# Optimization experiments

Measured on AMD Instinct MI355X. Metric: run time of the kernel, lower is better.

Reference implementation:

```python
import jax, jax.numpy as jnp
from jax import lax
import numpy as np

V, E, H, L = 512, 512, 1024, 2
B, T = 128, 512
PAD = 0


def _uniform(k, shape, bound):
    return jax.random.uniform(k, shape, jnp.float32, -bound, bound)


def setup_inputs() -> dict:
    key = jax.random.key(0)
    ks = jax.random.split(key, 14)
    kH = 1.0 / np.sqrt(H)
    inp = {
        'seq': jax.random.randint(ks[0], (B, T), 0, V, dtype=jnp.int32),
        'seq_lens': jax.random.randint(ks[1], (B,), 1, T + 1, dtype=jnp.int32),
        'teacher_p': jnp.asarray(0.5, jnp.float32),
        'embeds': jax.random.normal(ks[2], (V, E), jnp.float32),
        # layer 0: input size E; layer 1: input size H (PyTorch gate order i,f,g,o)
        'W_ih0': _uniform(ks[3], (4 * H, E), kH),
        'W_hh0': _uniform(ks[4], (4 * H, H), kH),
        'b_ih0': _uniform(ks[5], (4 * H,), kH),
        'b_hh0': _uniform(ks[6], (4 * H,), kH),
        'W_ih1': _uniform(ks[7], (4 * H, H), kH),
        'W_hh1': _uniform(ks[8], (4 * H, H), kH),
        'b_ih1': _uniform(ks[9], (4 * H,), kH),
        'b_hh1': _uniform(ks[10], (4 * H,), kH),
        'fc_w': _uniform(ks[11], (V, H), 1.0 / np.sqrt(H)),
        'fc_b': _uniform(ks[12], (V,), 1.0 / np.sqrt(H)),
    }
    return inp


def _lstm_cell(x, h, c, Wih, Whh, bih, bhh):
    g = x @ Wih.T + h @ Whh.T + (bih + bhh)  # [B, 4H]
    i, f, gg, o = jnp.split(g, 4, axis=-1)
    c = jax.nn.sigmoid(f) * c + jax.nn.sigmoid(i) * jnp.tanh(gg)
    h = jax.nn.sigmoid(o) * jnp.tanh(c)
    return h, c


def reference(seq, seq_lens, teacher_p, embeds, W_ih0, W_hh0, b_ih0, b_hh0,
              W_ih1, W_hh1, b_ih1, b_hh1, fc_w, fc_b):
    emb = embeds.at[PAD].set(0.0)  # padding_idx row is zero
    # pre-drawn teacher-forcing uniforms, one per (t, b)
    u = jax.random.uniform(jax.random.key(1), (T, B), jnp.float32)

    def step(carry, xs):
        h0, c0, h1, c1, prev_logits = carry
        tok_t, u_t, t = xs
        use_teacher = (t == 0) | (u_t < teacher_p)
        tok = jnp.where(use_teacher, tok_t, jnp.argmax(prev_logits, axis=1).astype(tok_t.dtype))
        x = emb[tok]  # [B, E]
        h0, c0 = _lstm_cell(x, h0, c0, W_ih0, W_hh0, b_ih0, b_hh0)
        h1, c1 = _lstm_cell(h0, h1, c1, W_ih1, W_hh1, b_ih1, b_hh1)
        logits = h1 @ fc_w.T + fc_b  # [B, V]
        return (h0, c0, h1, c1, logits), logits

    z = jnp.zeros((B, H), jnp.float32)
    init = (z, z, z, z, jnp.zeros((B, V), jnp.float32))
    xs = (seq.T, u, jnp.arange(T))
    _, logits = lax.scan(step, init, xs)  # [T, B, V]
    return jnp.transpose(logits, (1, 0, 2))  # [B, T, V]
```

## Files before the change

kernel.cpp:

```cpp
#include <hip/hip_runtime.h>
#include <cstdint>
#include <cstddef>

#define BB 128
#define TT 512
#define VV 512
#define EE 512
#define HH 1024
#define NBLK 256
#define BHS ((size_t)BB * HH)

__device__ __forceinline__ float tf_uniform(unsigned i) {
  unsigned x0 = 0u;
  unsigned x1 = i;
  const unsigned k0 = 0u, k1 = 1u, k2 = 0x1BD11BDBu;
  x0 += k0; x1 += k1;
#define ROTL_(v, r) (((v) << (r)) | ((v) >> (32 - (r))))
#define RND_(r) { x0 += x1; x1 = ROTL_(x1, (r)); x1 ^= x0; }
  RND_(13) RND_(15) RND_(26) RND_(6)   x0 += k1; x1 += k2 + 1u;
  RND_(17) RND_(29) RND_(16) RND_(24)  x0 += k2; x1 += k0 + 2u;
  RND_(13) RND_(15) RND_(26) RND_(6)   x0 += k0; x1 += k1 + 3u;
  RND_(17) RND_(29) RND_(16) RND_(24)  x0 += k1; x1 += k2 + 4u;
  RND_(13) RND_(15) RND_(26) RND_(6)   x0 += k2; x1 += k0 + 5u;
#undef RND_
#undef ROTL_
  unsigned bits = x0 ^ x1;
  unsigned fb = (bits >> 9) | 0x3f800000u;
  return __uint_as_float(fb) - 1.0f;
}

__device__ __forceinline__ void gridbar(unsigned* bar, unsigned target) {
  __syncthreads();
  if (threadIdx.x == 0) {
    __threadfence();
    __hip_atomic_fetch_add(bar, 1u, __ATOMIC_RELAXED, __HIP_MEMORY_SCOPE_AGENT);
    while (__hip_atomic_fetch_add(bar, 0u, __ATOMIC_RELAXED, __HIP_MEMORY_SCOPE_AGENT) < target) {
      __builtin_amdgcn_s_sleep(1);
    }
    __threadfence();
  }
  __syncthreads();
}

__global__ __launch_bounds__(256) void init_kernel(float* __restrict__ h0T,
                                                   float* __restrict__ c0T,
                                                   float* __restrict__ h1T,
                                                   float* __restrict__ c1T,
                                                   unsigned* __restrict__ bar) {
  int tid = blockIdx.x * 256 + threadIdx.x;
  if (tid == 0) *bar = 0u;
  if (tid < (int)BHS) {
    h0T[tid] = 0.f; c0T[tid] = 0.f; h1T[tid] = 0.f; c1T[tid] = 0.f;
  }
}

__global__ __launch_bounds__(256, 1) void lstm_persistent(
    const int* __restrict__ seq,
    const float* __restrict__ teacher_p,
    const float* __restrict__ emb,
    const float* __restrict__ Wih0, const float* __restrict__ Whh0,
    const float* __restrict__ bih0, const float* __restrict__ bhh0,
    const float* __restrict__ Wih1, const float* __restrict__ Whh1,
    const float* __restrict__ bih1, const float* __restrict__ bhh1,
    const float* __restrict__ fcw, const float* __restrict__ fcb,
    float* __restrict__ out,
    float* __restrict__ h0T, float* __restrict__ c0T,
    float* __restrict__ h1T, float* __restrict__ c1T,
    unsigned long long* __restrict__ fcpart,
    unsigned* __restrict__ bar) {
  __shared__ float Xs[32][132];
  __shared__ float Ws2[16][36];
  __shared__ float Xsf[64][36];
  __shared__ float Wsf[8][68];
  __shared__ int tok_s[BB];

  const int tid = threadIdx.x;
  const int bn  = blockIdx.x;
  const int ty  = tid >> 3;
  const int tx  = tid & 7;

  const float tp = teacher_p[0];

  float bc0[2][4], bc1[2][4];
#pragma unroll
  for (int r = 0; r < 2; ++r) {
    int j = (tid + (r << 8)) >> 7;
    int u = (bn << 2) + j;
#pragma unroll
    for (int g = 0; g < 4; ++g) {
      bc0[r][g] = bih0[g * HH + u] + bhh0[g * HH + u];
      bc1[r][g] = bih1[g * HH + u] + bhh1[g * HH + u];
    }
  }

  const int wc  = tid >> 3;
  const int wkq = tid & 7;
  const int gr  = (wc >> 2) * HH + (bn << 2) + (wc & 3);
  const float* wih0row = Wih0 + (size_t)gr * EE;
  const float* whh0row = Whh0 + (size_t)gr * HH;
  const float* wih1row = Wih1 + (size_t)gr * HH;
  const float* whh1row = Whh1 + (size_t)gr * HH;

  const int rb = bn >> 6, cb = bn & 63;
  const int fb = tid >> 3;
  const int fcc = tid & 7;
  const int fn = (cb << 3) + fcc;
  const float fcbr = fcb[fn];
  const float* fcwrow = fcw + (size_t)((cb << 3) + (tid >> 4)) * HH;

  unsigned target = 0;

  for (int t = 0; t < TT; ++t) {
    const float* h0r = h0T + (size_t)(t & 1) * BHS;
    float*       h0w = h0T + (size_t)((t + 1) & 1) * BHS;
    const float* h1r = h1T + (size_t)(t & 1) * BHS;
    float*       h1w = h1T + (size_t)((t + 1) & 1) * BHS;

    {
      int b = tid >> 1, h = tid & 1;
      unsigned long long best = 0ull;
      if (t > 0) {
        const unsigned long long* fp = fcpart + ((size_t)b << 6);
#pragma unroll 8
        for (int i = 0; i < 32; ++i) {
          unsigned long long k2 = fp[(i << 1) + h];
          if (k2 > best) best = k2;
        }
        unsigned long long o = __shfl_xor(best, 1);
        if (o > best) best = o;
      }
      if (h == 0) {
        int sel;
        if (t == 0) {
          sel = seq[(size_t)b * TT];
        } else {
          float uu = tf_uniform((unsigned)(t * BB + b));
          sel = (uu < tp) ? seq[(size_t)b * TT + t]
                          : (int)(0xFFFFFFFFu - (unsigned)(best & 0xFFFFFFFFull));
        }
        tok_s[b] = sel;
      }
    }
    __syncthreads();

    {
      float acc[4][2] = {{0.f,0.f},{0.f,0.f},{0.f,0.f},{0.f,0.f}};
      float4 x0, x1, x2, x3, w;

      auto pf = [&](int kt) {
        if (kt < 16) {
          const int kb = kt << 5;
          { int f=tid;     int b=f>>3, kq=f&7; int tk=tok_s[b];
            x0 = tk ? *(const float4*)(emb + ((size_t)tk<<9) + kb + (kq<<2)) : make_float4(0.f,0.f,0.f,0.f); }
          { int f=tid+256; int b=f>>3, kq=f&7; int tk=tok_s[b];
            x1 = tk ? *(const float4*)(emb + ((size_t)tk<<9) + kb + (kq<<2)) : make_float4(0.f,0.f,0.f,0.f); }
          { int f=tid+512; int b=f>>3, kq=f&7; int tk=tok_s[b];
            x2 = tk ? *(const float4*)(emb + ((size_t)tk<<9) + kb + (kq<<2)) : make_float4(0.f,0.f,0.f,0.f); }
          { int f=tid+768; int b=f>>3, kq=f&7; int tk=tok_s[b];
            x3 = tk ? *(const float4*)(emb + ((size_t)tk<<9) + kb + (kq<<2)) : make_float4(0.f,0.f,0.f,0.f); }
          if (tid < 128) w = *(const float4*)(wih0row + kb + (wkq<<2));
        } else {
          const float* src = h0r + ((size_t)(kt - 16) << 5) * BB;
          { int f=tid;     x0 = *(const float4*)(src + (f>>5)*BB + ((f&31)<<2)); }
          { int f=tid+256; x1 = *(const float4*)(src + (f>>5)*BB + ((f&31)<<2)); }
          { int f=tid+512; x2 = *(const float4*)(src + (f>>5)*BB + ((f&31)<<2)); }
          { int f=tid+768; x3 = *(const float4*)(src + (f>>5)*BB + ((f&31)<<2)); }
          if (tid < 128) w = *(const float4*)(whh0row + ((kt - 16) << 5) + (wkq<<2));
        }
      };
      auto st = [&](int kt) {
        if (kt < 16) {
          { int f=tid;     int b=f>>3, kk=(f&7)<<2; Xs[kk][b]=x0.x; Xs[kk+1][b]=x0.y; Xs[kk+2][b]=x0.z; Xs[kk+3][b]=x0.w; }
          { int f=tid+256; int b=f>>3, kk=(f&7)<<2; Xs[kk][b]=x1.x; Xs[kk+1][b]=x1.y; Xs[kk+2][b]=x1.z; Xs[kk+3][b]=x1.w; }
          { int f=tid+512; int b=f>>3, kk=(f&7)<<2; Xs[kk][b]=x2.x; Xs[kk+1][b]=x2.y; Xs[kk+2][b]=x2.z; Xs[kk+3][b]=x2.w; }
          { int f=tid+768; int b=f>>3, kk=(f&7)<<2; Xs[kk][b]=x3.x; Xs[kk+1][b]=x3.y; Xs[kk+2][b]=x3.z; Xs[kk+3][b]=x3.w; }
        } else {
          { int f=tid;     *(float4*)&Xs[f>>5][(f&31)<<2] = x0; }
          { int f=tid+256; *(float4*)&Xs[f>>5][(f&31)<<2] = x1; }
          { int f=tid+512; *(float4*)&Xs[f>>5][(f&31)<<2] = x2; }
          { int f=tid+768; *(float4*)&Xs[f>>5][(f&31)<<2] = x3; }
        }
        if (tid < 128) *(float4*)&Ws2[wc][wkq<<2] = w;
      };

      pf(0);
      for (int kt = 0; kt < 48; ++kt) {
        st(kt);
        __syncthreads();
        if (kt < 47) pf(kt + 1);
#pragma unroll
        for (int k4 = 0; k4 < 8; ++k4) {
          float w0[4], w1[4];
          *(float4*)w0 = *(const float4*)&Ws2[tx << 1][k4 << 2];
          *(float4*)w1 = *(const float4*)&Ws2[(tx << 1) + 1][k4 << 2];
#pragma unroll
          for (int kk = 0; kk < 4; ++kk) {
            float a[4];
            *(float4*)a = *(const float4*)&Xs[(k4 << 2) + kk][ty << 2];
#pragma unroll
            for (int i = 0; i < 4; ++i) {
              acc[i][0] = fmaf(a[i], w0[kk], acc[i][0]);
              acc[i][1] = fmaf(a[i], w1[kk], acc[i][1]);
            }
          }
        }
        __syncthreads();
      }

      float* gbuf = &Xs[0][0];
#pragma unroll
      for (int i = 0; i < 4; ++i) {
        int r = (ty << 2) + i;
        gbuf[r * 17 + (tx << 1)]     = acc[i][0];
        gbuf[r * 17 + (tx << 1) + 1] = acc[i][1];
      }
      __syncthreads();
#pragma unroll
      for (int r = 0; r < 2; ++r) {
        int idx = tid + (r << 8);
        int b = idx & 127, j = idx >> 7;
        float gi = gbuf[b * 17 + j]      + bc0[r][0];
        float gf = gbuf[b * 17 + 4 + j]  + bc0[r][1];
        float gg = gbuf[b * 17 + 8 + j]  + bc0[r][2];
        float go = gbuf[b * 17 + 12 + j] + bc0[r][3];
        float i_ = 1.f / (1.f + expf(-gi));
        float f_ = 1.f / (1.f + expf(-gf));
        float g_ = tanhf(gg);
        float o_ = 1.f / (1.f + expf(-go));
        size_t off = ((size_t)((bn << 2) + j)) * BB + b;
        float cn = f_ * c0T[off] + i_ * g_;
        c0T[off] = cn;
        h0w[off] = o_ * tanhf(cn);
      }
    }
    target += NBLK; gridbar(bar, target);

    {
      float acc[4][2] = {{0.f,0.f},{0.f,0.f},{0.f,0.f},{0.f,0.f}};
      float4 x0, x1, x2, x3, w;

      auto pf2 = [&](int kt) {
        const float* src = (kt < 32) ? (h0w + ((size_t)kt << 5) * BB)
                                     : (h1r + ((size_t)(kt - 32) << 5) * BB);
        { int f=tid;     x0 = *(const float4*)(src + (f>>5)*BB + ((f&31)<<2)); }
        { int f=tid+256; x1 = *(const float4*)(src + (f>>5)*BB + ((f&31)<<2)); }
        { int f=tid+512; x2 = *(const float4*)(src + (f>>5)*BB + ((f&31)<<2)); }
        { int f=tid+768; x3 = *(const float4*)(src + (f>>5)*BB + ((f&31)<<2)); }
        if (tid < 128) {
          w = (kt < 32) ? *(const float4*)(wih1row + (kt << 5) + (wkq<<2))
                        : *(const float4*)(whh1row + ((kt - 32) << 5) + (wkq<<2));
        }
      };
      auto st2 = [&]() {
        { int f=tid;     *(float4*)&Xs[f>>5][(f&31)<<2] = x0; }
        { int f=tid+256; *(float4*)&Xs[f>>5][(f&31)<<2] = x1; }
        { int f=tid+512; *(float4*)&Xs[f>>5][(f&31)<<2] = x2; }
        { int f=tid+768; *(float4*)&Xs[f>>5][(f&31)<<2] = x3; }
        if (tid < 128) *(float4*)&Ws2[wc][wkq<<2] = w;
      };

      pf2(0);
      for (int kt = 0; kt < 64; ++kt) {
        st2();
        __syncthreads();
        if (kt < 63) pf2(kt + 1);
#pragma unroll
        for (int k4 = 0; k4 < 8; ++k4) {
          float w0[4], w1[4];
          *(float4*)w0 = *(const float4*)&Ws2[tx << 1][k4 << 2];
          *(float4*)w1 = *(const float4*)&Ws2[(tx << 1) + 1][k4 << 2];
#pragma unroll
          for (int kk = 0; kk < 4; ++kk) {
            float a[4];
            *(float4*)a = *(const float4*)&Xs[(k4 << 2) + kk][ty << 2];
#pragma unroll
            for (int i = 0; i < 4; ++i) {
              acc[i][0] = fmaf(a[i], w0[kk], acc[i][0]);
              acc[i][1] = fmaf(a[i], w1[kk], acc[i][1]);
            }
          }
        }
        __syncthreads();
      }

      float* gbuf = &Xs[0][0];
#pragma unroll
      for (int i = 0; i < 4; ++i) {
        int r = (ty << 2) + i;
        gbuf[r * 17 + (tx << 1)]     = acc[i][0];
        gbuf[r * 17 + (tx << 1) + 1] = acc[i][1];
      }
      __syncthreads();
#pragma unroll
      for (int r = 0; r < 2; ++r) {
        int idx = tid + (r << 8);
        int b = idx & 127, j = idx >> 7;
        float gi = gbuf[b * 17 + j]      + bc1[r][0];
        float gf = gbuf[b * 17 + 4 + j]  + bc1[r][1];
        float gg = gbuf[b * 17 + 8 + j]  + bc1[r][2];
        float go = gbuf[b * 17 + 12 + j] + bc1[r][3];
        float i_ = 1.f / (1.f + expf(-gi));
        float f_ = 1.f / (1.f + expf(-gf));
        float g_ = tanhf(gg);
        float o_ = 1.f / (1.f + expf(-go));
        size_t off = ((size_t)((bn << 2) + j)) * BB + b;
        float cn = f_ * c1T[off] + i_ * g_;
        c1T[off] = cn;
        h1w[off] = o_ * tanhf(cn);
      }
    }
    target += NBLK; gridbar(bar, target);

    {
      float facc = 0.f;
      float4 y0, y1, fw;
      auto pf3 = [&](int kt) {
        const float* src = h1w + ((size_t)kt << 6) * BB + ((size_t)rb << 5);
        { int f=tid;     y0 = *(const float4*)(src + (f>>3)*BB + ((f&7)<<2)); }
        { int f=tid+256; y1 = *(const float4*)(src + (f>>3)*BB + ((f&7)<<2)); }
        if (tid < 128) fw = *(const float4*)(fcwrow + (kt << 6) + ((tid & 15) << 2));
      };
      auto st3 = [&]() {
        { int f=tid;     *(float4*)&Xsf[f>>3][(f&7)<<2] = y0; }
        { int f=tid+256; *(float4*)&Xsf[f>>3][(f&7)<<2] = y1; }
        if (tid < 128) *(float4*)&Wsf[tid >> 4][(tid & 15) << 2] = fw;
      };
      pf3(0);
      for (int kt = 0; kt < 16; ++kt) {
        st3();
        __syncthreads();
        if (kt < 15) pf3(kt + 1);
#pragma unroll
        for (int k = 0; k < 64; ++k)
          facc = fmaf(Xsf[k][fb], Wsf[fcc][k], facc);
        __syncthreads();
      }
      int b = (rb << 5) + fb;
      float lg = facc + fcbr;
      out[((size_t)b * TT + t) * VV + fn] = lg;
      unsigned sbits = __float_as_uint(lg);
      sbits = (sbits & 0x80000000u) ? ~sbits : (sbits | 0x80000000u);
      unsigned long long key = ((unsigned long long)sbits << 32) |
                               (unsigned long long)(0xFFFFFFFFu - (unsigned)fn);
#pragma unroll
      for (int off = 4; off > 0; off >>= 1) {
        unsigned long long o = __shfl_down(key, off, 8);
        if (o > key) key = o;
      }
      if (fcc == 0) fcpart[((size_t)b << 6) + cb] = key;
    }
    target += NBLK; gridbar(bar, target);
  }
}

extern "C" void kernel_launch(void* const* d_in, const int* in_sizes, int n_in,
                              void* d_out, int out_size, void* d_ws, size_t ws_size,
                              hipStream_t stream) {
  const int*   seq       = (const int*)d_in[0];
  const float* teacher_p = (const float*)d_in[2];
  const float* embeds    = (const float*)d_in[3];
  const float* W_ih0     = (const float*)d_in[4];
  const float* W_hh0     = (const float*)d_in[5];
  const float* b_ih0     = (const float*)d_in[6];
  const float* b_hh0     = (const float*)d_in[7];
  const float* W_ih1     = (const float*)d_in[8];
  const float* W_hh1     = (const float*)d_in[9];
  const float* b_ih1     = (const float*)d_in[10];
  const float* b_hh1     = (const float*)d_in[11];
  const float* fc_w      = (const float*)d_in[12];
  const float* fc_b      = (const float*)d_in[13];
  float* out = (float*)d_out;

  char* ws = (char*)d_ws;
  float* h0T = (float*)(ws);
  float* c0T = (float*)(ws + 2 * BHS * 4);
  float* h1T = (float*)(ws + 3 * BHS * 4);
  float* c1T = (float*)(ws + 5 * BHS * 4);
  unsigned long long* fcpart = (unsigned long long*)(ws + 6 * BHS * 4);
  unsigned* bar = (unsigned*)(ws + 6 * BHS * 4 + 65536);

  init_kernel<<<512, 256, 0, stream>>>(h0T, c0T, h1T, c1T, bar);

  void* args[] = {
    (void*)&seq, (void*)&teacher_p, (void*)&embeds,
    (void*)&W_ih0, (void*)&W_hh0, (void*)&b_ih0, (void*)&b_hh0,
    (void*)&W_ih1, (void*)&W_hh1, (void*)&b_ih1, (void*)&b_hh1,
    (void*)&fc_w, (void*)&fc_b, (void*)&out,
    (void*)&h0T, (void*)&c0T, (void*)&h1T, (void*)&c1T,
    (void*)&fcpart, (void*)&bar
  };
  hipError_t err = hipLaunchCooperativeKernel((void*)lstm_persistent,
                                              dim3(NBLK), dim3(256), args, 0, stream);
  if (err != hipSuccess) {
    lstm_persistent<<<dim3(NBLK), dim3(256), 0, stream>>>(
        seq, teacher_p, embeds, W_ih0, W_hh0, b_ih0, b_hh0,
        W_ih1, W_hh1, b_ih1, b_hh1, fc_w, fc_b, out,
        h0T, c0T, h1T, c1T, fcpart, bar);
  }
}
```

Baseline: 108.1 ms.

## Keep LSTM and FC weights register-resident in persistent kernel, stream activations

Each block now loads its slice of the gate and FC weight matrices into registers once before the time loop. Per step it streams only the batch activations through shared memory in row-major layout, with a split-K dot-product across warps reduced by shuffles and shared-memory partials. This removes the re-reading of roughly 40MB of weights from memory on every timestep. Block size goes to 512 threads, which raises register pressure (about 128 float registers for weights) and risks spills or lower occupancy.

```diff
diff --git a/kernel.cpp b/kernel.cpp
--- a/kernel.cpp
+++ b/kernel.cpp
@@ -8,6 +8,7 @@
 #define EE 512
 #define HH 1024
 #define NBLK 256
+#define NTHR 512
 #define BHS ((size_t)BB * HH)
 
 __device__ __forceinline__ float tf_uniform(unsigned i) {
@@ -29,6 +30,8 @@
   return __uint_as_float(fb) - 1.0f;
 }
 
+__device__ __forceinline__ float4 ld4(const float* p) { return *(const float4*)(p); }
+
 __device__ __forceinline__ void gridbar(unsigned* bar, unsigned target) {
   __syncthreads();
   if (threadIdx.x == 0) {
@@ -42,19 +45,14 @@
   __syncthreads();
 }
 
-__global__ __launch_bounds__(256) void init_kernel(float* __restrict__ h0T,
-                                                   float* __restrict__ c0T,
-                                                   float* __restrict__ h1T,
-                                                   float* __restrict__ c1T,
+__global__ __launch_bounds__(256) void init_kernel(float* __restrict__ wsf,
                                                    unsigned* __restrict__ bar) {
-  int tid = blockIdx.x * 256 + threadIdx.x;
+  size_t tid = (size_t)blockIdx.x * 256 + threadIdx.x;
   if (tid == 0) *bar = 0u;
-  if (tid < (int)BHS) {
-    h0T[tid] = 0.f; c0T[tid] = 0.f; h1T[tid] = 0.f; c1T[tid] = 0.f;
-  }
+  if (tid < 6 * BHS) wsf[tid] = 0.f;
 }
 
-__global__ __launch_bounds__(256, 1) void lstm_persistent(
+__global__ __launch_bounds__(NTHR, 2) void lstm_persistent(
     const int* __restrict__ seq,
     const float* __restrict__ teacher_p,
     const float* __restrict__ emb,
@@ -64,50 +62,60 @@
     const float* __restrict__ bih1, const float* __restrict__ bhh1,
     const float* __restrict__ fcw, const float* __restrict__ fcb,
     float* __restrict__ out,
-    float* __restrict__ h0T, float* __restrict__ c0T,
-    float* __restrict__ h1T, float* __restrict__ c1T,
+    float* __restrict__ h0T, float* __restrict__ c0,
+    float* __restrict__ h1T, float* __restrict__ c1,
     unsigned long long* __restrict__ fcpart,
     unsigned* __restrict__ bar) {
-  __shared__ float Xs[32][132];
-  __shared__ float Ws2[16][36];
-  __shared__ float Xsf[64][36];
-  __shared__ float Wsf[8][68];
-  __shared__ int tok_s[BB];
-
-  const int tid = threadIdx.x;
-  const int bn  = blockIdx.x;
-  const int ty  = tid >> 3;
-  const int tx  = tid & 7;
-
+  __shared__ float xbuf[8704];
+  __shared__ float gacc[BB][17];
+  __shared__ float scr[8][4][17];
+  __shared__ int   tok_s[BB];
+
+  const int tid   = threadIdx.x;
+  const int bn    = blockIdx.x;
+  const int w     = tid >> 6;
+  const int lane  = tid & 63;
+  const int c16   = lane & 15;
+  const int squad = lane >> 4;
+  const int s32   = (w << 2) | squad;
+  const int c8    = lane & 7;
+  const int oct   = lane >> 3;
+  const int s64   = (w << 3) | oct;
+  const int grow  = (c16 >> 2) * HH + (bn << 2) + (c16 & 3);
+  const int rb    = bn & 3, cb = bn >> 2;
+  const int ucell = (bn << 2) + (tid & 3);
+
+  float4 w0r[12], w1r[16], wfr[4];
+  {
+    const int k0 = s32 * 48;
+#pragma unroll
+    for (int q = 0; q < 12; ++q) {
+      int k = k0 + (q << 2);
+      w0r[q] = (k < EE) ? ld4(Wih0 + (size_t)grow * EE + k)
+                        : ld4(Whh0 + (size_t)grow * HH + (k - EE));
+    }
+  }
+  {
+    const int k0 = s32 * 64;
+#pragma unroll
+    for (int q = 0; q < 16; ++q) {
+      int k = k0 + (q << 2);
+      w1r[q] = (k < HH) ? ld4(Wih1 + (size_t)grow * HH + k)
+                        : ld4(Whh1 + (size_t)grow * HH + (k - HH));
+    }
+  }
+  {
+    const float* wrow = fcw + (size_t)((cb << 3) + c8) * HH + s64 * 16;
+#pragma unroll
+    for (int q = 0; q < 4; ++q) wfr[q] = ld4(wrow + (q << 2));
+  }
+  float bc0[4], bc1[4];
+#pragma unroll
+  for (int g = 0; g < 4; ++g) {
+    bc0[g] = bih0[g * HH + ucell] + bhh0[g * HH + ucell];
+    bc1[g] = bih1[g * HH + ucell] + bhh1[g * HH + ucell];
+  }
   const float tp = teacher_p[0];
-
-  float bc0[2][4], bc1[2][4];
-#pragma unroll
-  for (int r = 0; r < 2; ++r) {
-    int j = (tid + (r << 8)) >> 7;
-    int u = (bn << 2) + j;
-#pragma unroll
-    for (int g = 0; g < 4; ++g) {
-      bc0[r][g] = bih0[g * HH + u] + bhh0[g * HH + u];
-      bc1[r][g] = bih1[g * HH + u] + bhh1[g * HH + u];
-    }
-  }
-
-  const int wc  = tid >> 3;
-  const int wkq = tid & 7;
-  const int gr  = (wc >> 2) * HH + (bn << 2) + (wc & 3);
-  const float* wih0row = Wih0 + (size_t)gr * EE;
-  const float* whh0row = Whh0 + (size_t)gr * HH;
-  const float* wih1row = Wih1 + (size_t)gr * HH;
-  const float* whh1row = Whh1 + (size_t)gr * HH;
-
-  const int rb = bn >> 6, cb = bn & 63;
-  const int fb = tid >> 3;
-  const int fcc = tid & 7;
-  const int fn = (cb << 3) + fcc;
-  const float fcbr = fcb[fn];
-  const float* fcwrow = fcw + (size_t)((cb << 3) + (tid >> 4)) * HH;
-
   unsigned target = 0;
 
   for (int t = 0; t < TT; ++t) {
@@ -117,19 +125,21 @@
     float*       h1w = h1T + (size_t)((t + 1) & 1) * BHS;
 
     {
-      int b = tid >> 1, h = tid & 1;
+      int b = tid >> 2, qd = tid & 3;
       unsigned long long best = 0ull;
       if (t > 0) {
         const unsigned long long* fp = fcpart + ((size_t)b << 6);
-#pragma unroll 8
-        for (int i = 0; i < 32; ++i) {
-          unsigned long long k2 = fp[(i << 1) + h];
+#pragma unroll 4
+        for (int i = 0; i < 16; ++i) {
+          unsigned long long k2 = fp[(i << 2) + qd];
           if (k2 > best) best = k2;
         }
-        unsigned long long o = __shfl_xor(best, 1);
-        if (o > best) best = o;
-      }
-      if (h == 0) {
+        unsigned long long o1 = __shfl_xor(best, 1);
+        if (o1 > best) best = o1;
+        unsigned long long o2 = __shfl_xor(best, 2);
+        if (o2 > best) best = o2;
+      }
+      if (qd == 0) {
         int sel;
         if (t == 0) {
           sel = seq[(size_t)b * TT];
@@ -144,210 +154,225 @@
     __syncthreads();
 
     {
-      float acc[4][2] = {{0.f,0.f},{0.f,0.f},{0.f,0.f},{0.f,0.f}};
-      float4 x0, x1, x2, x3, w;
-
-      auto pf = [&](int kt) {
-        if (kt < 16) {
-          const int kb = kt << 5;
-          { int f=tid;     int b=f>>3, kq=f&7; int tk=tok_s[b];
-            x0 = tk ? *(const float4*)(emb + ((size_t)tk<<9) + kb + (kq<<2)) : make_float4(0.f,0.f,0.f,0.f); }
-          { int f=tid+256; int b=f>>3, kq=f&7; int tk=tok_s[b];
-            x1 = tk ? *(const float4*)(emb + ((size_t)tk<<9) + kb + (kq<<2)) : make_float4(0.f,0.f,0.f,0.f); }
-          { int f=tid+512; int b=f>>3, kq=f&7; int tk=tok_s[b];
-            x2 = tk ? *(const float4*)(emb + ((size_t)tk<<9) + kb + (kq<<2)) : make_float4(0.f,0.f,0.f,0.f); }
-          { int f=tid+768; int b=f>>3, kq=f&7; int tk=tok_s[b];
-            x3 = tk ? *(const float4*)(emb + ((size_t)tk<<9) + kb + (kq<<2)) : make_float4(0.f,0.f,0.f,0.f); }
-          if (tid < 128) w = *(const float4*)(wih0row + kb + (wkq<<2));
-        } else {
-          const float* src = h0r + ((size_t)(kt - 16) << 5) * BB;
-          { int f=tid;     x0 = *(const float4*)(src + (f>>5)*BB + ((f&31)<<2)); }
-          { int f=tid+256; x1 = *(const float4*)(src + (f>>5)*BB + ((f&31)<<2)); }
-          { int f=tid+512; x2 = *(const float4*)(src + (f>>5)*BB + ((f&31)<<2)); }
-          { int f=tid+768; x3 = *(const float4*)(src + (f>>5)*BB + ((f&31)<<2)); }
-          if (tid < 128) w = *(const float4*)(whh0row + ((kt - 16) << 5) + (wkq<<2));
-        }
-      };
-      auto st = [&](int kt) {
-        if (kt < 16) {
-          { int f=tid;     int b=f>>3, kk=(f&7)<<2; Xs[kk][b]=x0.x; Xs[kk+1][b]=x0.y; Xs[kk+2][b]=x0.z; Xs[kk+3][b]=x0.w; }
-          { int f=tid+256; int b=f>>3, kk=(f&7)<<2; Xs[kk][b]=x1.x; Xs[kk+1][b]=x1.y; Xs[kk+2][b]=x1.z; Xs[kk+3][b]=x1.w; }
-          { int f=tid+512; int b=f>>3, kk=(f&7)<<2; Xs[kk][b]=x2.x; Xs[kk+1][b]=x2.y; Xs[kk+2][b]=x2.z; Xs[kk+3][b]=x2.w; }
-          { int f=tid+768; int b=f>>3, kk=(f&7)<<2; Xs[kk][b]=x3.x; Xs[kk+1][b]=x3.y; Xs[kk+2][b]=x3.z; Xs[kk+3][b]=x3.w; }
-        } else {
-          { int f=tid;     *(float4*)&Xs[f>>5][(f&31)<<2] = x0; }
-          { int f=tid+256; *(float4*)&Xs[f>>5][(f&31)<<2] = x1; }
-          { int f=tid+512; *(float4*)&Xs[f>>5][(f&31)<<2] = x2; }
-          { int f=tid+768; *(float4*)&Xs[f>>5][(f&31)<<2] = x3; }
-        }
-        if (tid < 128) *(float4*)&Ws2[wc][wkq<<2] = w;
-      };
-
-      pf(0);
-      for (int kt = 0; kt < 48; ++kt) {
-        st(kt);
-        __syncthreads();
-        if (kt < 47) pf(kt + 1);
-#pragma unroll
-        for (int k4 = 0; k4 < 8; ++k4) {
-          float w0[4], w1[4];
-          *(float4*)w0 = *(const float4*)&Ws2[tx << 1][k4 << 2];
-          *(float4*)w1 = *(const float4*)&Ws2[(tx << 1) + 1][k4 << 2];
-#pragma unroll
-          for (int kk = 0; kk < 4; ++kk) {
-            float a[4];
-            *(float4*)a = *(const float4*)&Xs[(k4 << 2) + kk][ty << 2];
-#pragma unroll
-            for (int i = 0; i < 4; ++i) {
-              acc[i][0] = fmaf(a[i], w0[kk], acc[i][0]);
-              acc[i][1] = fmaf(a[i], w1[kk], acc[i][1]);
-            }
+      float4 sg[3];
+      auto loadP1 = [&](int bt) {
+#pragma unroll
+        for (int i = 0; i < 3; ++i) {
+          int u = tid + (i << 9);
+          int row = u / 384;
+          int k = (u - row * 384) << 2;
+          int b = (bt << 2) + row;
+          float4 v;
+          if (k < EE) {
+            int tk = tok_s[b];
+            v = tk ? ld4(emb + (size_t)tk * EE + k) : make_float4(0.f, 0.f, 0.f, 0.f);
+          } else {
+            v = ld4(h0r + (size_t)b * HH + (k - EE));
           }
-        }
-        __syncthreads();
-      }
-
-      float* gbuf = &Xs[0][0];
-#pragma unroll
-      for (int i = 0; i < 4; ++i) {
-        int r = (ty << 2) + i;
-        gbuf[r * 17 + (tx << 1)]     = acc[i][0];
-        gbuf[r * 17 + (tx << 1) + 1] = acc[i][1];
-      }
-      __syncthreads();
-#pragma unroll
-      for (int r = 0; r < 2; ++r) {
-        int idx = tid + (r << 8);
-        int b = idx & 127, j = idx >> 7;
-        float gi = gbuf[b * 17 + j]      + bc0[r][0];
-        float gf = gbuf[b * 17 + 4 + j]  + bc0[r][1];
-        float gg = gbuf[b * 17 + 8 + j]  + bc0[r][2];
-        float go = gbuf[b * 17 + 12 + j] + bc0[r][3];
+          sg[i] = v;
+        }
+      };
+      auto writeP1 = [&]() {
+#pragma unroll
+        for (int i = 0; i < 3; ++i) {
+          int u = tid + (i << 9);
+          int row = u / 384;
+          int k = (u - row * 384) << 2;
+          int dst = row * 1664 + (k / 48) * 52 + (k % 48);
+          *(float4*)(xbuf + dst) = sg[i];
+        }
+      };
+      loadP1(0); writeP1(); __syncthreads();
+      for (int bt = 0; bt < 32; ++bt) {
+        if (bt < 31) loadP1(bt + 1);
+        const float* xp0 = xbuf + s32 * 52;
+#pragma unroll 2
+        for (int r = 0; r < 4; ++r) {
+          const float* xp = xp0 + r * 1664;
+          float a0 = 0.f, a1 = 0.f, a2 = 0.f, a3 = 0.f;
+#pragma unroll
+          for (int q = 0; q < 12; ++q) {
+            float4 xv = *(const float4*)(xp + (q << 2));
+            a0 = fmaf(xv.x, w0r[q].x, a0);
+            a1 = fmaf(xv.y, w0r[q].y, a1);
+            a2 = fmaf(xv.z, w0r[q].z, a2);
+            a3 = fmaf(xv.w, w0r[q].w, a3);
+          }
+          float acc = (a0 + a1) + (a2 + a3);
+          acc += __shfl_xor(acc, 16);
+          acc += __shfl_xor(acc, 32);
+          if (squad == 0) scr[w][r][c16] = acc;
+        }
+        __syncthreads();
+        if (tid < 64) {
+          int r = tid >> 4, c = tid & 15;
+          float s = 0.f;
+#pragma unroll
+          for (int ww = 0; ww < 8; ++ww) s += scr[ww][r][c];
+          gacc[(bt << 2) + r][c] = s;
+        }
+        if (bt < 31) writeP1();
+        __syncthreads();
+      }
+      {
+        int b = tid >> 2, j = tid & 3;
+        float gi = gacc[b][j]      + bc0[0];
+        float gf = gacc[b][4 + j]  + bc0[1];
+        float gg = gacc[b][8 + j]  + bc0[2];
+        float go = gacc[b][12 + j] + bc0[3];
         float i_ = 1.f / (1.f + expf(-gi));
         float f_ = 1.f / (1.f + expf(-gf));
         float g_ = tanhf(gg);
         float o_ = 1.f / (1.f + expf(-go));
-        size_t off = ((size_t)((bn << 2) + j)) * BB + b;
-        float cn = f_ * c0T[off] + i_ * g_;
-        c0T[off] = cn;
+        size_t off = (size_t)b * HH + ucell;
+        float cn = f_ * c0[off] + i_ * g_;
+        c0[off] = cn;
         h0w[off] = o_ * tanhf(cn);
       }
     }
     target += NBLK; gridbar(bar, target);
 
     {
-      float acc[4][2] = {{0.f,0.f},{0.f,0.f},{0.f,0.f},{0.f,0.f}};
-      float4 x0, x1, x2, x3, w;
-
-      auto pf2 = [&](int kt) {
-        const float* src = (kt < 32) ? (h0w + ((size_t)kt << 5) * BB)
-                                     : (h1r + ((size_t)(kt - 32) << 5) * BB);
-        { int f=tid;     x0 = *(const float4*)(src + (f>>5)*BB + ((f&31)<<2)); }
-        { int f=tid+256; x1 = *(const float4*)(src + (f>>5)*BB + ((f&31)<<2)); }
-        { int f=tid+512; x2 = *(const float4*)(src + (f>>5)*BB + ((f&31)<<2)); }
-        { int f=tid+768; x3 = *(const float4*)(src + (f>>5)*BB + ((f&31)<<2)); }
-        if (tid < 128) {
-          w = (kt < 32) ? *(const float4*)(wih1row + (kt << 5) + (wkq<<2))
-                        : *(const float4*)(whh1row + ((kt - 32) << 5) + (wkq<<2));
-        }
-      };
-      auto st2 = [&]() {
-        { int f=tid;     *(float4*)&Xs[f>>5][(f&31)<<2] = x0; }
-        { int f=tid+256; *(float4*)&Xs[f>>5][(f&31)<<2] = x1; }
-        { int f=tid+512; *(float4*)&Xs[f>>5][(f&31)<<2] = x2; }
-        { int f=tid+768; *(float4*)&Xs[f>>5][(f&31)<<2] = x3; }
-        if (tid < 128) *(float4*)&Ws2[wc][wkq<<2] = w;
-      };
-
-      pf2(0);
-      for (int kt = 0; kt < 64; ++kt) {
-        st2();
-        __syncthreads();
-        if (kt < 63) pf2(kt + 1);
-#pragma unroll
-        for (int k4 = 0; k4 < 8; ++k4) {
-          float w0[4], w1[4];
-          *(float4*)w0 = *(const float4*)&Ws2[tx << 1][k4 << 2];
-          *(float4*)w1 = *(const float4*)&Ws2[(tx << 1) + 1][k4 << 2];
-#pragma unroll
-          for (int kk = 0; kk < 4; ++kk) {
-            float a[4];
-            *(float4*)a = *(const float4*)&Xs[(k4 << 2) + kk][ty << 2];
-#pragma unroll
-            for (int i = 0; i < 4; ++i) {
-              acc[i][0] = fmaf(a[i], w0[kk], acc[i][0]);
-              acc[i][1] = fmaf(a[i], w1[kk], acc[i][1]);
-            }
+      float4 sg[4];
+      auto loadP2 = [&](int bt) {
+#pragma unroll
+        for (int i = 0; i < 4; ++i) {
+          int u = tid + (i << 9);
+          int row = u >> 9;
+          int k = (u & 511) << 2;
+          int b = (bt << 2) + row;
+          sg[i] = (k < HH) ? ld4(h0w + (size_t)b * HH + k)
+                           : ld4(h1r + (size_t)b * HH + (k - HH));
+        }
+      };
+      auto writeP2 = [&]() {
+#pragma unroll
+        for (int i = 0; i < 4; ++i) {
+          int u = tid + (i << 9);
+          int row = u >> 9;
+          int k = (u & 511) << 2;
+          int dst = row * 2176 + (k >> 6) * 68 + (k & 63);
+          *(float4*)(xbuf + dst) = sg[i];
+        }
+      };
+      loadP2(0); writeP2(); __syncthreads();
+      for (int bt = 0; bt < 32; ++bt) {
+        if (bt < 31) loadP2(bt + 1);
+        const float* xp0 = xbuf + s32 * 68;
+#pragma unroll 2
+        for (int r = 0; r < 4; ++r) {
+          const float* xp = xp0 + r * 2176;
+          float a0 = 0.f, a1 = 0.f, a2 = 0.f, a3 = 0.f;
+#pragma unroll
+          for (int q = 0; q < 16; ++q) {
+            float4 xv = *(const float4*)(xp + (q << 2));
+            a0 = fmaf(xv.x, w1r[q].x, a0);
+            a1 = fmaf(xv.y, w1r[q].y, a1);
+            a2 = fmaf(xv.z, w1r[q].z, a2);
+            a3 = fmaf(xv.w, w1r[q].w, a3);
           }
-        }
-        __syncthreads();
-      }
-
-      float* gbuf = &Xs[0][0];
-#pragma unroll
-      for (int i = 0; i < 4; ++i) {
-        int r = (ty << 2) + i;
-        gbuf[r * 17 + (tx << 1)]     = acc[i][0];
-        gbuf[r * 17 + (tx << 1) + 1] = acc[i][1];
-      }
-      __syncthreads();
-#pragma unroll
-      for (int r = 0; r < 2; ++r) {
-        int idx = tid + (r << 8);
-        int b = idx & 127, j = idx >> 7;
-        float gi = gbuf[b * 17 + j]      + bc1[r][0];
-        float gf = gbuf[b * 17 + 4 + j]  + bc1[r][1];
-        float gg = gbuf[b * 17 + 8 + j]  + bc1[r][2];
-        float go = gbuf[b * 17 + 12 + j] + bc1[r][3];
+          float acc = (a0 + a1) + (a2 + a3);
+          acc += __shfl_xor(acc, 16);
+          acc += __shfl_xor(acc, 32);
+          if (squad == 0) scr[w][r][c16] = acc;
+        }
+        __syncthreads();
+        if (tid < 64) {
+          int r = tid >> 4, c = tid & 15;
+          float s = 0.f;
+#pragma unroll
+          for (int ww = 0; ww < 8; ++ww) s += scr[ww][r][c];
+          gacc[(bt << 2) + r][c] = s;
+        }
+        if (bt < 31) writeP2();
+        __syncthreads();
+      }
+      {
+        int b = tid >> 2, j = tid & 3;
+        float gi = gacc[b][j]      + bc1[0];
+        float gf = gacc[b][4 + j]  + bc1[1];
+        float gg = gacc[b][8 + j]  + bc1[2];
+        float go = gacc[b][12 + j] + bc1[3];
         float i_ = 1.f / (1.f + expf(-gi));
         float f_ = 1.f / (1.f + expf(-gf));
         float g_ = tanhf(gg);
         float o_ = 1.f / (1.f + expf(-go));
-        size_t off = ((size_t)((bn << 2) + j)) * BB + b;
-        float cn = f_ * c1T[off] + i_ * g_;
-        c1T[off] = cn;
+        size_t off = (size_t)b * HH + ucell;
+        float cn = f_ * c1[off] + i_ * g_;
+        c1[off] = cn;
         h1w[off] = o_ * tanhf(cn);
       }
     }
     target += NBLK; gridbar(bar, target);
 
     {
-      float facc = 0.f;
-      float4 y0, y1, fw;
-      auto pf3 = [&](int kt) {
-        const float* src = h1w + ((size_t)kt << 6) * BB + ((size_t)rb << 5);
-        { int f=tid;     y0 = *(const float4*)(src + (f>>3)*BB + ((f&7)<<2)); }
-        { int f=tid+256; y1 = *(const float4*)(src + (f>>3)*BB + ((f&7)<<2)); }
-        if (tid < 128) fw = *(const float4*)(fcwrow + (kt << 6) + ((tid & 15) << 2));
-      };
-      auto st3 = [&]() {
-        { int f=tid;     *(float4*)&Xsf[f>>3][(f&7)<<2] = y0; }
-        { int f=tid+256; *(float4*)&Xsf[f>>3][(f&7)<<2] = y1; }
-        if (tid < 128) *(float4*)&Wsf[tid >> 4][(tid & 15) << 2] = fw;
-      };
-      pf3(0);
-      for (int kt = 0; kt < 16; ++kt) {
-        st3();
-        __syncthreads();
-        if (kt < 15) pf3(kt + 1);
-#pragma unroll
-        for (int k = 0; k < 64; ++k)
-          facc = fmaf(Xsf[k][fb], Wsf[fcc][k], facc);
-        __syncthreads();
-      }
-      int b = (rb << 5) + fb;
-      float lg = facc + fcbr;
-      out[((size_t)b * TT + t) * VV + fn] = lg;
-      unsigned sbits = __float_as_uint(lg);
-      sbits = (sbits & 0x80000000u) ? ~sbits : (sbits | 0x80000000u);
-      unsigned long long key = ((unsigned long long)sbits << 32) |
-                               (unsigned long long)(0xFFFFFFFFu - (unsigned)fn);
-#pragma unroll
-      for (int off = 4; off > 0; off >>= 1) {
-        unsigned long long o = __shfl_down(key, off, 8);
-        if (o > key) key = o;
-      }
-      if (fcc == 0) fcpart[((size_t)b << 6) + cb] = key;
+      float4 sg[2];
+      auto loadF = [&](int bt) {
+#pragma unroll
+        for (int i = 0; i < 2; ++i) {
+          int u = tid + (i << 9);
+          int row = u >> 8;
+          int k = (u & 255) << 2;
+          int b = (rb << 5) + (bt << 2) + row;
+          sg[i] = ld4(h1w + (size_t)b * HH + k);
+        }
+      };
+      auto writeF = [&]() {
+#pragma unroll
+        for (int i = 0; i < 2; ++i) {
+          int u = tid + (i << 9);
+          int row = u >> 8;
+          int k = (u & 255) << 2;
+          int dst = row * 1280 + (k >> 4) * 20 + (k & 15);
+          *(float4*)(xbuf + dst) = sg[i];
+        }
+      };
+      loadF(0); writeF(); __syncthreads();
+      for (int bt = 0; bt < 8; ++bt) {
+        if (bt < 7) loadF(bt + 1);
+        const float* xp0 = xbuf + s64 * 20;
+#pragma unroll 2
+        for (int r = 0; r < 4; ++r) {
+          const float* xp = xp0 + r * 1280;
+          float a0 = 0.f, a1 = 0.f, a2 = 0.f, a3 = 0.f;
+#pragma unroll
+          for (int q = 0; q < 4; ++q) {
+            float4 xv = *(const float4*)(xp + (q << 2));
+            a0 = fmaf(xv.x, wfr[q].x, a0);
+            a1 = fmaf(xv.y, wfr[q].y, a1);
+            a2 = fmaf(xv.z, wfr[q].z, a2);
+            a3 = fmaf(xv.w, wfr[q].w, a3);
+          }
+          float acc = (a0 + a1) + (a2 + a3);
+          acc += __shfl_xor(acc, 8);
+          acc += __shfl_xor(acc, 16);
+          acc += __shfl_xor(acc, 32);
+          if (oct == 0) scr[w][r][c8] = acc;
+        }
+        __syncthreads();
+        if (tid < 32) {
+          int r = tid >> 3, c = tid & 7;
+          float s = 0.f;
+#pragma unroll
+          for (int ww = 0; ww < 8; ++ww) s += scr[ww][r][c];
+          int n = (cb << 3) + c;
+          float lg = s + fcb[n];
+          int b = (rb << 5) + (bt << 2) + r;
+          out[((size_t)b * TT + t) * VV + n] = lg;
+          unsigned sbits = __float_as_uint(lg);
+          sbits = (sbits & 0x80000000u) ? ~sbits : (sbits | 0x80000000u);
+          unsigned long long key = ((unsigned long long)sbits << 32) |
+                                   (unsigned long long)(0xFFFFFFFFu - (unsigned)n);
+#pragma unroll
+          for (int off = 4; off > 0; off >>= 1) {
+            unsigned long long o = __shfl_down(key, off, 8);
+            if (o > key) key = o;
+          }
+          if (c == 0) fcpart[((size_t)b << 6) + cb] = key;
+        }
+        if (bt < 7) writeF();
+        __syncthreads();
+      }
     }
     target += NBLK; gridbar(bar, target);
   }
@@ -372,29 +397,29 @@
   float* out = (float*)d_out;
 
   char* ws = (char*)d_ws;
-  float* h0T = (float*)(ws);
-  float* c0T = (float*)(ws + 2 * BHS * 4);
-  float* h1T = (float*)(ws + 3 * BHS * 4);
-  float* c1T = (float*)(ws + 5 * BHS * 4);
+  float* h0 = (float*)(ws);
+  float* c0 = (float*)(ws + 2 * BHS * 4);
+  float* h1 = (float*)(ws + 3 * BHS * 4);
+  float* c1 = (float*)(ws + 5 * BHS * 4);
   unsigned long long* fcpart = (unsigned long long*)(ws + 6 * BHS * 4);
   unsigned* bar = (unsigned*)(ws + 6 * BHS * 4 + 65536);
 
-  init_kernel<<<512, 256, 0, stream>>>(h0T, c0T, h1T, c1T, bar);
+  init_kernel<<<3072, 256, 0, stream>>>((float*)ws, bar);
 
   void* args[] = {
     (void*)&seq, (void*)&teacher_p, (void*)&embeds,
     (void*)&W_ih0, (void*)&W_hh0, (void*)&b_ih0, (void*)&b_hh0,
     (void*)&W_ih1, (void*)&W_hh1, (void*)&b_ih1, (void*)&b_hh1,
     (void*)&fc_w, (void*)&fc_b, (void*)&out,
-    (void*)&h0T, (void*)&c0T, (void*)&h1T, (void*)&c1T,
+    (void*)&h0, (void*)&c0, (void*)&h1, (void*)&c1,
     (void*)&fcpart, (void*)&bar
   };
   hipError_t err = hipLaunchCooperativeKernel((void*)lstm_persistent,
-                                              dim3(NBLK), dim3(256), args, 0, stream);
+                                              dim3(NBLK), dim3(NTHR), args, 0, stream);
   if (err != hipSuccess) {
-    lstm_persistent<<<dim3(NBLK), dim3(256), 0, stream>>>(
+    lstm_persistent<<<dim3(NBLK), dim3(NTHR), 0, stream>>>(
         seq, teacher_p, embeds, W_ih0, W_hh0, b_ih0, b_hh0,
         W_ih1, W_hh1, b_ih1, b_hh1, fc_w, fc_b, out,
-        h0T, c0T, h1T, c1T, fcpart, bar);
+        h0, c0, h1, c1, fcpart, bar);
   }
 }
```

After: 119.2 ms. 10.3% more time.
